# Performance work log

Measured on AMD Instinct MI355X. Metric: run time of the kernel, lower is better.

## Reference

```python
import jax, jax.numpy as jnp
import numpy as np

N = 64
K_CHEB = 5
EPS = 1e-5

# db4 decomposition filters (scaling_filter.mat Lo_D / Hi_D, length 8)
_LO = np.array([-0.010597401784997278, 0.032883011666982945, 0.030841381835986965,
                -0.18703481171888114, -0.02798376941698385, 0.6308807679295904,
                0.7148465705525415, 0.23037781330885523], dtype=np.float32)
_HI = np.array([-0.23037781330885523, 0.7148465705525415, -0.6308807679295904,
                -0.02798376941698385, 0.18703481171888114, 0.030841381835986965,
                0.032883011666982945, -0.010597401784997278], dtype=np.float32)
# torch stores np.flip(filters) and Conv2d does cross-correlation -> use flipped taps here too
_KERN = np.stack([_LO[::-1], _HI[::-1]])[:, None, None, :].copy()  # [2,1,1,8]


def _wavelet_step(x):
    # x: [B, C, 1, W]; circular pad 3 each side, depthwise len-8 conv, stride 2
    p = 3  # filter_length // 2 - 1
    xp = jnp.concatenate([x[..., -p:], x, x[..., :p]], axis=-1)
    b, c, h, wp = xp.shape
    out = jax.lax.conv_general_dilated(
        xp.reshape(b * c, 1, h, wp), jnp.asarray(_KERN), (1, 2), 'VALID',
        dimension_numbers=('NCHW', 'OIHW', 'NCHW'))
    out = out.reshape(b, c, 2, h, -1)
    return out[:, :, 0], out[:, :, 1]  # (approx, detail)


def _cbam(x, fc1, fc2, sa_w):
    # x: [B, 657, 1, 64]; channel attention then spatial attention
    def mlp(v):  # v: [B, C, 1, 1]
        h = jax.nn.relu(jnp.einsum('oc,bchw->bohw', fc1, v))
        return jnp.einsum('oc,bchw->bohw', fc2, h)
    avg = x.mean(axis=(2, 3), keepdims=True)
    mx = x.max(axis=(2, 3), keepdims=True)
    x = x * jax.nn.sigmoid(mlp(avg) + mlp(mx))
    s = jnp.concatenate([x.mean(axis=1, keepdims=True), x.max(axis=1, keepdims=True)], axis=1)
    sa = jax.nn.sigmoid(jax.lax.conv_general_dilated(
        s, sa_w, (1, 1), ((3, 3), (3, 3)), dimension_numbers=('NCHW', 'OIHW', 'NCHW')))
    return x * sa


def _global_edge_weight(w_tril, mask):
    xs, ys = np.tril_indices(N)
    E = jnp.zeros((N, N), w_tril.dtype).at[xs, ys].set(w_tril)
    E = E + E.T - jnp.diag(jnp.diag(E))
    return (E * mask).reshape(-1)


def _norm_adj(edges, w):
    # PyG NewSGConv.norm: add remaining self-loops (fill=1), deg from |w|, sym normalize
    row, col = edges[0], edges[1]
    has_self = jnp.zeros((N,), w.dtype).at[row].add(jnp.where(row == col, 1.0, 0.0)) > 0
    w_self = jnp.where(has_self, 0.0, 1.0).astype(w.dtype)
    deg = jnp.zeros((N,), w.dtype).at[row].add(jnp.abs(w)) + w_self
    dsafe = jnp.where(deg > 0, deg, 1.0)
    dinv = jnp.where(deg > 0, jax.lax.rsqrt(dsafe), 0.0)
    norm = dinv[row] * w * dinv[col]
    A = jnp.zeros((N, N), w.dtype).at[col, row].add(norm)  # out[i] = sum_j A[i,j] x[j]
    return A + jnp.diag(dinv * w_self * dinv)


def _gcn_block(x, A, W, b, g, be):
    # x: [B, N, C_in]; K-hop SGConv propagation, linear, train-mode batchnorm over (B, N)
    for _ in range(K_CHEB):
        x = jnp.einsum('ij,bjc->bic', A, x)
    x = x @ W.T + b
    mean = x.mean(axis=(0, 1))
    var = x.var(axis=(0, 1))
    return (x - mean) * jax.lax.rsqrt(var + EPS) * g + be


def _classify(x, W1, b1, g, be, W2, b2):
    out = x.reshape(x.shape[0], -1) @ W1.T + b1
    out = (out - out.mean(0)) * jax.lax.rsqrt(out.var(0) + EPS) * g + be
    return jax.nn.log_softmax(out @ W2.T + b2, axis=1)


def _forward(x, local_graph_weight, global_mask, ca_fc1, ca_fc2, sa_conv, edge_weight_tril,
             ld_W, ld_b, ld_g, ld_be, ld1_W, ld1_b, ld1_g, ld1_be,
             d_W, d_b, d_g, d_be, d1_W, d1_b, d1_g, d1_be,
             cls_W1, cls_b1, cls_g, cls_be, cls_W2, cls_b2, edges):
    xc = jnp.transpose(x, (0, 3, 2, 1))        # [B, 657, 1, 64]
    xc = _cbam(xc, ca_fc1, ca_fc2, sa_conv)
    xh = jnp.transpose(xc, (0, 3, 2, 1))       # [B, 64, 1, 657]
    # fi = floor(log2(200)) = 7 -> 4 decomposition levels: 657->328->164->82->41
    out1, _gamma = _wavelet_step(xh)
    out2, _beta = _wavelet_step(out1)
    out3, _alpha = _wavelet_step(out2)
    delta, _theta = _wavelet_step(out3)        # [B, 64, 1, 41]
    delta = delta[:, :, 0, :]                  # squeeze -> [B, 64, 41]
    gw = _global_edge_weight(edge_weight_tril, global_mask)
    A_loc = _norm_adj(edges, local_graph_weight)
    A_glb = _norm_adj(edges, gw)
    lf = _gcn_block(delta, A_loc, ld_W, ld_b, ld_g, ld_be)
    lf = _gcn_block(lf, A_loc, ld1_W, ld1_b, ld1_g, ld1_be)
    gf = _gcn_block(delta, A_glb, d_W, d_b, d_g, d_be)
    gf = _gcn_block(gf, A_glb, d1_W, d1_b, d1_g, d1_be)
    feat = jnp.concatenate([lf.mean(-1, keepdims=True), gf.mean(-1, keepdims=True)], axis=2)  # [B,64,2]
    return _classify(feat, cls_W1, cls_b1, cls_g, cls_be, cls_W2, cls_b2)


def setup_inputs() -> dict:
    key = jax.random.key(0)
    ks = iter(jax.random.split(key, 16))
    B = 512
    f32 = jnp.float32
    def rn(shape, s=0.05):
        return jax.random.normal(next(ks), shape, f32) * s
    ii = jnp.arange(N, dtype=jnp.int32)
    edges = jnp.stack([jnp.repeat(ii, N), jnp.tile(ii, N)])  # full 64x64 mesh (incl. self loops)
    return dict(
        x=jax.random.normal(next(ks), (B, N, 1, 657), f32),
        local_graph_weight=jax.random.uniform(next(ks), (N * N,), f32),
        global_mask=jnp.ones((N, N), f32),
        ca_fc1=rn((82, 657)),
        ca_fc2=rn((657, 82)),
        sa_conv=rn((1, 2, 7, 7), 0.1),
        edge_weight_tril=jax.random.uniform(next(ks), (N * (N + 1) // 2,), f32),
        ld_W=rn((16, 41)), ld_b=jnp.zeros(16, f32), ld_g=jnp.ones(16, f32), ld_be=jnp.zeros(16, f32),
        ld1_W=rn((4, 16)), ld1_b=jnp.zeros(4, f32), ld1_g=jnp.ones(4, f32), ld1_be=jnp.zeros(4, f32),
        d_W=rn((16, 41)), d_b=jnp.zeros(16, f32), d_g=jnp.ones(16, f32), d_be=jnp.zeros(16, f32),
        d1_W=rn((4, 16)), d1_b=jnp.zeros(4, f32), d1_g=jnp.ones(4, f32), d1_be=jnp.zeros(4, f32),
        cls_W1=rn((32, 128)), cls_b1=jnp.zeros(32, f32), cls_g=jnp.ones(32, f32), cls_be=jnp.zeros(32, f32),
        cls_W2=rn((2, 32)), cls_b2=jnp.zeros(2, f32),
        edges=edges,
    )


def reference(x, local_graph_weight, global_mask, ca_fc1, ca_fc2, sa_conv, edge_weight_tril,
              ld_W, ld_b, ld_g, ld_be, ld1_W, ld1_b, ld1_g, ld1_be,
              d_W, d_b, d_g, d_be, d1_W, d1_b, d1_g, d1_be,
              cls_W1, cls_b1, cls_g, cls_be, cls_W2, cls_b2, edges):
    return _forward(x, local_graph_weight, global_mask, ca_fc1, ca_fc2, sa_conv, edge_weight_tril,
                    ld_W, ld_b, ld_g, ld_be, ld1_W, ld1_b, ld1_g, ld1_be,
                    d_W, d_b, d_g, d_be, d1_W, d1_b, d1_g, d1_be,
                    cls_W1, cls_b1, cls_g, cls_be, cls_W2, cls_b2, edges)
```

## Files before the change

### kernel.cpp

```cpp
#include <hip/hip_runtime.h>
#include <math.h>

#define NB 512
#define NN 64
#define TL 657
#define LV1 328
#define LV2 164
#define LV3 82
#define LV4 41
#define HID 82
#define BAND 219
#define ST 66

#define WS_M      0
#define WS_ACC    32768
#define WS_SMEAN  36864
#define WS_SMAX   167936
#define WS_FC2T   299008
#define WS_H      514560
#define WS_CSUM   682496
#define WS_CMAX   2028032
#define WS_CATT   3373568
#define WS_Y1     682496
#define WS_DELTA  4876800
#define WS_Y2     4876800
#define WS_OUT1   5925376

#define ACC_Y1 0
#define ACC_Y2 64
#define ACC_O1 80

__device__ __forceinline__ float sigmoidf_(float v){ return 1.0f/(1.0f+expf(-v)); }

__device__ __forceinline__ void wav_level(float* __restrict__ dst, const float* __restrict__ src,
                                          int outL, int inL, int lane){
  const float DLO[8] = {0.23037781330885523f, 0.7148465705525415f, 0.6308807679295904f,
                        -0.02798376941698385f, -0.18703481171888114f, 0.030841381835986965f,
                        0.032883011666982945f, -0.010597401784997278f};
  for (int k=lane; k<outL; k+=64){
    int i0 = 2*k - 3;
    float a = 0.f;
    #pragma unroll
    for (int j=0;j<8;j++){
      int idx = i0 + j;
      idx = (idx < 0) ? idx + inL : ((idx >= inL) ? idx - inL : idx);
      a += src[idx]*DLO[j];
    }
    dst[k] = a;
  }
}

__device__ __forceinline__ void mm8(float* __restrict__ D, int dstride,
                                    const float* __restrict__ A, const float* __restrict__ Bm){
  int tid = threadIdx.x;
  int wv = tid >> 6, lane = tid & 63;
  int i0 = wv*8;
  float acc8[8];
  #pragma unroll
  for (int i=0;i<8;i++) acc8[i]=0.f;
  #pragma unroll
  for (int kc=0; kc<4; kc++){
    float bb[16];
    #pragma unroll
    for (int j=0;j<16;j++) bb[j] = Bm[(kc*16+j)*ST + lane];
    #pragma unroll
    for (int i=0;i<8;i++){
      const float2* ar = (const float2*)&A[(i0+i)*ST + kc*16];
      float s0=0.f, s1=0.f;
      #pragma unroll
      for (int j2=0;j2<8;j2++){
        float2 v = ar[j2];
        s0 += v.x*bb[2*j2]; s1 += v.y*bb[2*j2+1];
      }
      acc8[i] += s0+s1;
    }
  }
  #pragma unroll
  for (int i=0;i<8;i++) D[(i0+i)*dstride + lane] = acc8[i];
}

__global__ __launch_bounds__(512) void k_graph(
    const float* __restrict__ lgw, const float* __restrict__ gmask,
    const float* __restrict__ tril, const int* __restrict__ edges,
    const float* __restrict__ fc2,
    float* __restrict__ Mout, float* __restrict__ fc2T,
    double* __restrict__ acc)
{
  __shared__ float smem[3*NN*ST];
  __shared__ float deg[64], hs[64], dinv[64], wself[64];
  int tid = threadIdx.x;

  if (blockIdx.x >= 2){
    int gi = blockIdx.x - 2;
    int r0 = gi*83;
    int rn = (gi==7) ? (TL - 7*83) : 83;
    for (int i=tid; i<rn*HID; i+=512){
      int r = i / HID, u = i - r*HID;
      smem[u*85 + r] = fc2[(size_t)r0*HID + i];
    }
    __syncthreads();
    for (int j=tid; j<HID*83; j+=512){
      int u = j / 83, c = j - u*83;
      if (c < rn) fc2T[u*TL + r0 + c] = smem[u*85 + c];
    }
    return;
  }

  float* Wbuf = smem;
  float* Amat = smem + NN*ST;
  float* P1   = smem + 2*NN*ST;
  int g = blockIdx.x;
  if (g==0){ for (int i=tid;i<512;i+=512) acc[i]=0.0; }
  for (int e=tid;e<4096;e+=512){
    float w;
    if (g==0) w = lgw[e];
    else {
      int i=e>>6, j=e&63;
      int aa = (i>j)? i:j, bb = (i>j)? j:i;
      w = tril[aa*(aa+1)/2 + bb] * gmask[e];
    }
    Wbuf[e] = w;
  }
  for (int i=tid;i<NN*ST;i+=512) Amat[i] = 0.f;
  if (tid<64){ deg[tid]=0.f; hs[tid]=0.f; }
  __syncthreads();
  {
    int e0 = tid*8;
    int runr = edges[e0];
    float runv = 0.f;
    #pragma unroll 4
    for (int i=0;i<8;i++){
      int e = e0+i;
      int r = edges[e];
      int c = edges[4096+e];
      float w = Wbuf[e];
      if (r != runr){ atomicAdd(&deg[runr], runv); runr = r; runv = 0.f; }
      runv += fabsf(w);
      if (r == c) hs[r] = 1.f;
    }
    atomicAdd(&deg[runr], runv);
  }
  __syncthreads();
  if (tid<64){
    float w_ = (hs[tid] > 0.f) ? 0.f : 1.f;
    float d = deg[tid] + w_;
    dinv[tid] = (d > 0.f) ? rsqrtf(d) : 0.f;
    wself[tid] = w_;
  }
  __syncthreads();
  for (int e=tid;e<4096;e+=512){
    int r = edges[e], c = edges[4096+e];
    float nm = dinv[r]*Wbuf[e]*dinv[c];
    atomicAdd(&Amat[c*ST+r], nm);
  }
  __syncthreads();
  if (tid<64) Amat[tid*ST+tid] += dinv[tid]*wself[tid]*dinv[tid];
  __syncthreads();
  mm8(P1,   ST, Amat, Amat); __syncthreads();
  mm8(Wbuf, ST, P1,   P1);   __syncthreads();
  mm8(&Mout[g*4096], 64, Wbuf, Amat);
}

__global__ __launch_bounds__(256) void k_stats(
    const float* __restrict__ x,
    float* __restrict__ csum, float* __restrict__ cmax)
{
  int tid = threadIdx.x, b = blockIdx.x, band = blockIdx.y;
  if (tid >= BAND) return;
  int col = band*BAND + tid;
  const float* p = x + (size_t)b*NN*TL + col;
  float s = 0.f, m = -INFINITY;
  for (int n=0;n<NN;n+=16){
    float v0 = p[0*TL],  v1 = p[1*TL],  v2 = p[2*TL],  v3 = p[3*TL];
    float v4 = p[4*TL],  v5 = p[5*TL],  v6 = p[6*TL],  v7 = p[7*TL];
    float v8 = p[8*TL],  v9 = p[9*TL],  vA = p[10*TL], vB = p[11*TL];
    float vC = p[12*TL], vD = p[13*TL], vE = p[14*TL], vF = p[15*TL];
    p += 16*TL;
    s += ((v0+v1)+(v2+v3)) + ((v4+v5)+(v6+v7)) + ((v8+v9)+(vA+vB)) + ((vC+vD)+(vE+vF));
    float m01 = fmaxf(fmaxf(v0,v1), fmaxf(v2,v3));
    float m23 = fmaxf(fmaxf(v4,v5), fmaxf(v6,v7));
    float m45 = fmaxf(fmaxf(v8,v9), fmaxf(vA,vB));
    float m67 = fmaxf(fmaxf(vC,vD), fmaxf(vE,vF));
    m = fmaxf(m, fmaxf(fmaxf(m01,m23), fmaxf(m45,m67)));
  }
  csum[(size_t)b*TL + col] = s;
  cmax[(size_t)b*TL + col] = m;
}

__global__ __launch_bounds__(256) void k_mlp1(
    const float* __restrict__ csum, const float* __restrict__ cmax,
    const float* __restrict__ fc1, float* __restrict__ H)
{
  int tid = threadIdx.x, b = blockIdx.x, half = blockIdx.y;
  int wv = tid>>6, lane = tid&63;
  float s[11], m[11];
  #pragma unroll
  for (int i=0;i<11;i++){
    int c = lane + 64*i;
    bool ok = c < TL;
    s[i] = ok ? csum[(size_t)b*TL+c] : 0.f;
    m[i] = ok ? cmax[(size_t)b*TL+c] : 0.f;
  }
  int oend = half*41 + 41; if (oend > HID) oend = HID;
  for (int o = half*41 + wv; o < oend; o += 4){
    const float* fr = fc1 + (size_t)o*TL;
    float a = 0.f, bm = 0.f;
    #pragma unroll
    for (int i=0;i<11;i++){
      int c = lane + 64*i;
      float f = (c<TL) ? fr[c] : 0.f;
      a += f*s[i]; bm += f*m[i];
    }
    #pragma unroll
    for (int off=32;off;off>>=1){
      a  += __shfl_xor(a,off);
      bm += __shfl_xor(bm,off);
    }
    if (lane==0)
      H[(size_t)b*HID + o] = fmaxf(a*(1.0f/64.0f),0.f) + fmaxf(bm,0.f);
  }
}

__global__ __launch_bounds__(256) void k_mlp2(
    const float* __restrict__ H, const float* __restrict__ fc2T,
    float* __restrict__ catt)
{
  __shared__ float h[HID];
  int tid = threadIdx.x, b = blockIdx.x;
  if (tid < HID) h[tid] = H[(size_t)b*HID + tid];
  __syncthreads();
  int c0 = tid, c1 = tid+256, c2 = tid+512;
  bool ok2 = c2 < TL;
  float a0=0.f, a1=0.f, a2=0.f;
  #pragma unroll 2
  for (int u=0;u<HID;u++){
    const float* fr = fc2T + (size_t)u*TL;
    float hv = h[u];
    a0 += fr[c0]*hv;
    a1 += fr[c1]*hv;
    if (ok2) a2 += fr[c2]*hv;
  }
  size_t base = (size_t)b*TL;
  catt[base+c0] = sigmoidf_(a0);
  catt[base+c1] = sigmoidf_(a1);
  if (ok2) catt[base+c2] = sigmoidf_(a2);
}

__global__ __launch_bounds__(256) void k_wav(
    const float* __restrict__ x, const float* __restrict__ catt_g,
    float* __restrict__ delta, float* __restrict__ smean, float* __restrict__ smax)
{
  __shared__ float catt[TL];
  __shared__ float yb[4][TL];
  __shared__ float o1b[4][LV1];
  __shared__ float o2b[4][LV2];
  __shared__ float o3b[4][LV3];
  int tid = threadIdx.x, b = blockIdx.x;
  for (int i=tid;i<TL;i+=256) catt[i] = catt_g[(size_t)b*TL + i];
  __syncthreads();
  int wv = tid>>6, lane = tid&63;
  int n = blockIdx.y*4 + wv;
  float* y  = yb[wv];
  float* p1 = o1b[wv];
  float* p2 = o2b[wv];
  float* p3 = o3b[wv];
  const float DLO[8] = {0.23037781330885523f, 0.7148465705525415f, 0.6308807679295904f,
                        -0.02798376941698385f, -0.18703481171888114f, 0.030841381835986965f,
                        0.032883011666982945f, -0.010597401784997278f};
  const float* row = x + ((size_t)b*NN + n)*TL;
  float ls = 0.f, lm = -INFINITY;
  #pragma unroll
  for (int i=0;i<11;i++){
    int t = lane + 64*i;
    if (t < TL){
      float v = row[t]*catt[t];
      y[t] = v; ls += v; lm = fmaxf(lm,v);
    }
  }
  #pragma unroll
  for (int off=32;off;off>>=1){
    ls += __shfl_xor(ls,off);
    lm = fmaxf(lm, __shfl_xor(lm,off));
  }
  if (lane==0){ smean[b*NN+n] = ls*(1.0f/657.0f); smax[b*NN+n] = lm; }
  wav_level(p1, y,  LV1, TL,  lane);
  wav_level(p2, p1, LV2, LV1, lane);
  wav_level(p3, p2, LV3, LV2, lane);
  if (lane < LV4){
    int i0 = 2*lane - 3;
    float a = 0.f;
    #pragma unroll
    for (int j=0;j<8;j++){
      int idx = i0 + j;
      idx = (idx < 0) ? idx + LV3 : ((idx >= LV3) ? idx - LV3 : idx);
      a += p3[idx]*DLO[j];
    }
    delta[((size_t)b*NN + n)*LV4 + lane] = a;
  }
}

__global__ __launch_bounds__(256) void k_gcn1(
  const float* __restrict__ delta, const float* __restrict__ Mmat,
  const float* __restrict__ smean, const float* __restrict__ smax,
  const float* __restrict__ saw,
  const float* __restrict__ ldW, const float* __restrict__ ldb,
  const float* __restrict__ dW, const float* __restrict__ db2,
  float* __restrict__ Y1, double* __restrict__ acc)
{
  __shared__ float Dl[NN*LV4];
  __shared__ float Tt[NN*16];
  __shared__ float Mm[4096];
  __shared__ float Wl[16*LV4];
  __shared__ float satt[NN];
  __shared__ double red[256];
  int tid=threadIdx.x, b=blockIdx.x;
  if (tid < NN){
    float a = 0.f;
    #pragma unroll
    for (int kw=0;kw<7;kw++){
      int w = tid + kw - 3;
      if (0<=w && w<NN) a += smean[b*NN+w]*saw[21+kw] + smax[b*NN+w]*saw[70+kw];
    }
    satt[tid] = sigmoidf_(a);
  }
  __syncthreads();
  const float* ds = delta + (size_t)b*NN*LV4;
  for (int i=tid;i<NN*LV4;i+=256) Dl[i] = ds[i]*satt[i/LV4];
  for (int g=0; g<2; g++){
    const float* Ws = g ? dW : ldW;
    const float* bs = g ? db2 : ldb;
    for (int i=tid;i<16*LV4;i+=256) Wl[i]=Ws[i];
    for (int i=tid;i<4096;i+=256) Mm[i]=Mmat[g*4096+i];
    __syncthreads();
    for (int e=tid;e<NN*16;e+=256){
      int n=e>>4, o=e&15;
      const float* dr=&Dl[n*LV4];
      const float* wr=&Wl[o*LV4];
      float a=0.f;
      #pragma unroll 8
      for (int c=0;c<LV4;c++) a += dr[c]*wr[c];
      Tt[e]=a;
    }
    __syncthreads();
    float bias = bs[tid&15];
    float ps=0.f, pq=0.f;
    for (int m=0;m<4;m++){
      int e=tid+256*m;
      int n=e>>4, o=e&15;
      float a=bias;
      #pragma unroll 8
      for (int k=0;k<64;k++) a += Mm[n*64+k]*Tt[k*16+o];
      Y1[((size_t)b*NN+n)*32 + g*16 + o] = a;
      ps += a; pq += a*a;
    }
    red[tid]=(double)ps;
    __syncthreads();
    if (tid<16){ double t=0; for (int r=tid;r<256;r+=16) t+=red[r]; atomicAdd(&acc[ACC_Y1+g*32+tid], t); }
    __syncthreads();
    red[tid]=(double)pq;
    __syncthreads();
    if (tid<16){ double t=0; for (int r=tid;r<256;r+=16) t+=red[r]; atomicAdd(&acc[ACC_Y1+g*32+16+tid], t); }
    __syncthreads();
  }
}

__global__ __launch_bounds__(256) void k_gcn2(
  const float* __restrict__ Y1, const float* __restrict__ Mmat,
  const float* __restrict__ ldg, const float* __restrict__ ldbe,
  const float* __restrict__ dg, const float* __restrict__ dbe,
  const float* __restrict__ ld1W, const float* __restrict__ ld1b,
  const float* __restrict__ d1W, const float* __restrict__ d1b,
  float* __restrict__ Y2, double* __restrict__ acc)
{
  __shared__ float Yl[NN*32];
  __shared__ float T2[NN*8];
  __shared__ float Mm[2*4096];
  __shared__ float scl[32], sht[32];
  __shared__ double red[256];
  int tid=threadIdx.x, b=blockIdx.x;
  const float* ys = Y1 + (size_t)b*NN*32;
  for (int i=tid;i<NN*32;i+=256) Yl[i]=ys[i];
  for (int i=tid;i<8192;i+=256) Mm[i]=Mmat[i];
  if (tid<32){
    int g=tid>>4, o=tid&15;
    double s=acc[ACC_Y1+g*32+o], q=acc[ACC_Y1+g*32+16+o];
    double mean=s/32768.0;
    double var=q/32768.0 - mean*mean;
    float gam = g? dg[o] : ldg[o];
    float bet = g? dbe[o] : ldbe[o];
    float sc = gam * rsqrtf((float)var + 1e-5f);
    scl[tid]=sc; sht[tid]=bet - (float)mean*sc;
  }
  __syncthreads();
  for (int i=tid;i<NN*32;i+=256){ int c=i&31; Yl[i]=Yl[i]*scl[c]+sht[c]; }
  __syncthreads();
  for (int e=tid;e<NN*8;e+=256){
    int n=e>>3, c=e&7, g=c>>2, p=c&3;
    const float* w = (g? d1W : ld1W) + p*16;
    const float* yr = &Yl[n*32 + g*16];
    float a=0.f;
    #pragma unroll
    for (int o=0;o<16;o++) a += yr[o]*w[o];
    T2[e]=a;
  }
  __syncthreads();
  float ps=0.f,pq=0.f;
  for (int m=0;m<2;m++){
    int e=tid+256*m;
    int n=e>>3, c=e&7, g=c>>2;
    float a = g? d1b[c&3] : ld1b[c&3];
    const float* mr=&Mm[g*4096+n*64];
    #pragma unroll 8
    for (int k=0;k<64;k++) a += mr[k]*T2[k*8+c];
    Y2[((size_t)b*NN+n)*8 + c] = a;
    ps+=a; pq+=a*a;
  }
  red[tid]=(double)ps; __syncthreads();
  if (tid<8){ double t=0; for (int r=tid;r<256;r+=8) t+=red[r]; atomicAdd(&acc[ACC_Y2 + (tid>>2)*8 + (tid&3)], t); }
  __syncthreads();
  red[tid]=(double)pq; __syncthreads();
  if (tid<8){ double t=0; for (int r=tid;r<256;r+=8) t+=red[r]; atomicAdd(&acc[ACC_Y2 + (tid>>2)*8 + 4 + (tid&3)], t); }
}

__global__ __launch_bounds__(64) void k_featcls(
  const float* __restrict__ Y2,
  const float* __restrict__ ld1g, const float* __restrict__ ld1be,
  const float* __restrict__ d1g, const float* __restrict__ d1be,
  const float* __restrict__ W1, const float* __restrict__ b1,
  float* __restrict__ out1, double* __restrict__ acc)
{
  __shared__ float f[128];
  __shared__ float scl[8], sht[8];
  int tid=threadIdx.x, b=blockIdx.x;
  if (tid<8){
    int g=tid>>2, p=tid&3;
    double s=acc[ACC_Y2+g*8+p], q=acc[ACC_Y2+g*8+4+p];
    double mean=s/32768.0;
    double var=q/32768.0-mean*mean;
    float gam = g? d1g[p]:ld1g[p];
    float bet = g? d1be[p]:ld1be[p];
    float sc = gam*rsqrtf((float)var+1e-5f);
    scl[tid]=sc; sht[tid]=bet-(float)mean*sc;
  }
  __syncthreads();
  {
    const float* yr = Y2 + ((size_t)b*NN+tid)*8;
    float lf=0.f, gf=0.f;
    #pragma unroll
    for (int p=0;p<4;p++){
      lf += yr[p]*scl[p]+sht[p];
      gf += yr[4+p]*scl[4+p]+sht[4+p];
    }
    f[2*tid]   = lf*0.25f;
    f[2*tid+1] = gf*0.25f;
  }
  __syncthreads();
  if (tid<32){
    const float* w = W1 + tid*128;
    float a = b1[tid];
    #pragma unroll 4
    for (int m=0;m<128;m++) a += w[m]*f[m];
    out1[b*32+tid]=a;
    atomicAdd(&acc[ACC_O1+tid], (double)a);
    atomicAdd(&acc[ACC_O1+32+tid], (double)(a*a));
  }
}

__global__ __launch_bounds__(64) void k_cls2(
  const float* __restrict__ out1,
  const float* __restrict__ cg, const float* __restrict__ cbe,
  const float* __restrict__ W2, const float* __restrict__ b2,
  const double* __restrict__ acc, float* __restrict__ out)
{
  __shared__ float v[32];
  __shared__ float z[2];
  int tid=threadIdx.x, b=blockIdx.x;
  if (tid<32){
    double s=acc[ACC_O1+tid], q=acc[ACC_O1+32+tid];
    double mean=s/512.0;
    double var=q/512.0-mean*mean;
    float sc=cg[tid]*rsqrtf((float)var+1e-5f);
    float sh=cbe[tid]-(float)mean*sc;
    v[tid]=out1[b*32+tid]*sc+sh;
  }
  __syncthreads();
  if (tid<2){
    const float* w=W2+tid*32;
    float a=b2[tid];
    #pragma unroll
    for (int j=0;j<32;j++) a += w[j]*v[j];
    z[tid]=a;
  }
  __syncthreads();
  if (tid<2){
    float m=fmaxf(z[0],z[1]);
    float l=m+logf(expf(z[0]-m)+expf(z[1]-m));
    out[b*2+tid]=z[tid]-l;
  }
}

extern "C" void kernel_launch(void* const* d_in, const int* in_sizes, int n_in,
                              void* d_out, int out_size, void* d_ws, size_t ws_size,
                              hipStream_t stream) {
  (void)in_sizes; (void)n_in; (void)out_size; (void)ws_size;
  const float* x     = (const float*)d_in[0];
  const float* lgw   = (const float*)d_in[1];
  const float* gmask = (const float*)d_in[2];
  const float* fc1   = (const float*)d_in[3];
  const float* fc2   = (const float*)d_in[4];
  const float* saw   = (const float*)d_in[5];
  const float* tril  = (const float*)d_in[6];
  const float* ldW   = (const float*)d_in[7];
  const float* ldb   = (const float*)d_in[8];
  const float* ldg   = (const float*)d_in[9];
  const float* ldbe  = (const float*)d_in[10];
  const float* ld1W  = (const float*)d_in[11];
  const float* ld1b  = (const float*)d_in[12];
  const float* ld1g  = (const float*)d_in[13];
  const float* ld1be = (const float*)d_in[14];
  const float* dW    = (const float*)d_in[15];
  const float* db2   = (const float*)d_in[16];
  const float* dg    = (const float*)d_in[17];
  const float* dbe   = (const float*)d_in[18];
  const float* d1W   = (const float*)d_in[19];
  const float* d1b   = (const float*)d_in[20];
  const float* d1g   = (const float*)d_in[21];
  const float* d1be  = (const float*)d_in[22];
  const float* cW1   = (const float*)d_in[23];
  const float* cb1   = (const float*)d_in[24];
  const float* cgam  = (const float*)d_in[25];
  const float* cbet  = (const float*)d_in[26];
  const float* cW2   = (const float*)d_in[27];
  const float* cb2   = (const float*)d_in[28];
  const int*   edges = (const int*)d_in[29];

  char* ws = (char*)d_ws;
  float*  M     = (float*)(ws + WS_M);
  double* acc   = (double*)(ws + WS_ACC);
  float*  smean = (float*)(ws + WS_SMEAN);
  float*  smax  = (float*)(ws + WS_SMAX);
  float*  fc2T  = (float*)(ws + WS_FC2T);
  float*  Hbuf  = (float*)(ws + WS_H);
  float*  csum  = (float*)(ws + WS_CSUM);
  float*  cmax  = (float*)(ws + WS_CMAX);
  float*  catt  = (float*)(ws + WS_CATT);
  float*  Y1    = (float*)(ws + WS_Y1);
  float*  delta = (float*)(ws + WS_DELTA);
  float*  Y2    = (float*)(ws + WS_Y2);
  float*  out1  = (float*)(ws + WS_OUT1);
  float*  out   = (float*)d_out;

  k_graph<<<10, 512, 0, stream>>>(lgw, gmask, tril, edges, fc2, M, fc2T, acc);
  k_stats<<<dim3(NB, 3), 256, 0, stream>>>(x, csum, cmax);
  k_mlp1<<<dim3(NB, 2), 256, 0, stream>>>(csum, cmax, fc1, Hbuf);
  k_mlp2<<<NB, 256, 0, stream>>>(Hbuf, fc2T, catt);
  k_wav<<<dim3(NB, 16), 256, 0, stream>>>(x, catt, delta, smean, smax);
  k_gcn1<<<NB, 256, 0, stream>>>(delta, M, smean, smax, saw, ldW, ldb, dW, db2, Y1, acc);
  k_gcn2<<<NB, 256, 0, stream>>>(Y1, M, ldg, ldbe, dg, dbe, ld1W, ld1b, d1W, d1b, Y2, acc);
  k_featcls<<<NB, 64, 0, stream>>>(Y2, ld1g, ld1be, d1g, d1be, cW1, cb1, out1, acc);
  k_cls2<<<NB, 64, 0, stream>>>(out1, cgam, cbet, cW2, cb2, acc, out);
}
```

Baseline: 188.3 us.

## Fuse graph setup with channel stats and merge the two MLP kernels

The graph/fc2-transpose blocks are merged into the channel-stats kernel as extra blocks of a single launch, and the two channel-attention MLP stages are fused into one kernel that keeps the hidden vector in shared memory. This removes two kernel launches and the global round trip through the hidden buffer. The graph blocks now share a launch with the stats blocks, which may change the overlap, and stats blocks use 512-thread launches with about 329 active threads. The mlp kernel now handles one batch per block rather than splitting the hidden layer across two blocks.

Result: faster. 183.0 us (-2.9%).

```diff
diff --git a/kernel.cpp b/kernel.cpp
--- a/kernel.cpp
+++ b/kernel.cpp
@@ -9,7 +9,6 @@
 #define LV3 82
 #define LV4 41
 #define HID 82
-#define BAND 219
 #define ST 66
 
 #define WS_M      0
@@ -17,7 +16,6 @@
 #define WS_SMEAN  36864
 #define WS_SMAX   167936
 #define WS_FC2T   299008
-#define WS_H      514560
 #define WS_CSUM   682496
 #define WS_CMAX   2028032
 #define WS_CATT   3373568
@@ -79,21 +77,51 @@
   for (int i=0;i<8;i++) D[(i0+i)*dstride + lane] = acc8[i];
 }
 
-__global__ __launch_bounds__(512) void k_graph(
+__global__ __launch_bounds__(512) void k_front(
+    const float* __restrict__ x,
     const float* __restrict__ lgw, const float* __restrict__ gmask,
     const float* __restrict__ tril, const int* __restrict__ edges,
     const float* __restrict__ fc2,
+    float* __restrict__ csum, float* __restrict__ cmax,
     float* __restrict__ Mout, float* __restrict__ fc2T,
     double* __restrict__ acc)
 {
   __shared__ float smem[3*NN*ST];
   __shared__ float deg[64], hs[64], dinv[64], wself[64];
   int tid = threadIdx.x;
-
-  if (blockIdx.x >= 2){
-    int gi = blockIdx.x - 2;
-    int r0 = gi*83;
-    int rn = (gi==7) ? (TL - 7*83) : 83;
+  int bid = blockIdx.x;
+
+  if (bid < 2*NB){
+    int b = bid >> 1, band = bid & 1;
+    int c0   = band ? 329 : 0;
+    int len  = band ? 328 : 329;
+    if (tid >= len) return;
+    int col = c0 + tid;
+    const float* p = x + (size_t)b*NN*TL + col;
+    float s = 0.f, m = -INFINITY;
+    for (int n=0;n<NN;n+=16){
+      float v0 = p[0*TL],  v1 = p[1*TL],  v2 = p[2*TL],  v3 = p[3*TL];
+      float v4 = p[4*TL],  v5 = p[5*TL],  v6 = p[6*TL],  v7 = p[7*TL];
+      float v8 = p[8*TL],  v9 = p[9*TL],  vA = p[10*TL], vB = p[11*TL];
+      float vC = p[12*TL], vD = p[13*TL], vE = p[14*TL], vF = p[15*TL];
+      p += 16*TL;
+      s += ((v0+v1)+(v2+v3)) + ((v4+v5)+(v6+v7)) + ((v8+v9)+(vA+vB)) + ((vC+vD)+(vE+vF));
+      float m01 = fmaxf(fmaxf(v0,v1), fmaxf(v2,v3));
+      float m23 = fmaxf(fmaxf(v4,v5), fmaxf(v6,v7));
+      float m45 = fmaxf(fmaxf(v8,v9), fmaxf(vA,vB));
+      float m67 = fmaxf(fmaxf(vC,vD), fmaxf(vE,vF));
+      m = fmaxf(m, fmaxf(fmaxf(m01,m23), fmaxf(m45,m67)));
+    }
+    csum[(size_t)b*TL + col] = s;
+    cmax[(size_t)b*TL + col] = m;
+    return;
+  }
+
+  int gi = bid - 2*NB;
+  if (gi >= 2){
+    int t8 = gi - 2;
+    int r0 = t8*83;
+    int rn = (t8==7) ? (TL - 7*83) : 83;
     for (int i=tid; i<rn*HID; i+=512){
       int r = i / HID, u = i - r*HID;
       smem[u*85 + r] = fc2[(size_t)r0*HID + i];
@@ -109,8 +137,8 @@
   float* Wbuf = smem;
   float* Amat = smem + NN*ST;
   float* P1   = smem + 2*NN*ST;
-  int g = blockIdx.x;
-  if (g==0){ for (int i=tid;i<512;i+=512) acc[i]=0.0; }
+  int g = gi;
+  if (g==0 && tid<512) acc[tid]=0.0;
   for (int e=tid;e<4096;e+=512){
     float w;
     if (g==0) w = lgw[e];
@@ -161,55 +189,30 @@
   mm8(&Mout[g*4096], 64, Wbuf, Amat);
 }
 
-__global__ __launch_bounds__(256) void k_stats(
-    const float* __restrict__ x,
-    float* __restrict__ csum, float* __restrict__ cmax)
-{
-  int tid = threadIdx.x, b = blockIdx.x, band = blockIdx.y;
-  if (tid >= BAND) return;
-  int col = band*BAND + tid;
-  const float* p = x + (size_t)b*NN*TL + col;
-  float s = 0.f, m = -INFINITY;
-  for (int n=0;n<NN;n+=16){
-    float v0 = p[0*TL],  v1 = p[1*TL],  v2 = p[2*TL],  v3 = p[3*TL];
-    float v4 = p[4*TL],  v5 = p[5*TL],  v6 = p[6*TL],  v7 = p[7*TL];
-    float v8 = p[8*TL],  v9 = p[9*TL],  vA = p[10*TL], vB = p[11*TL];
-    float vC = p[12*TL], vD = p[13*TL], vE = p[14*TL], vF = p[15*TL];
-    p += 16*TL;
-    s += ((v0+v1)+(v2+v3)) + ((v4+v5)+(v6+v7)) + ((v8+v9)+(vA+vB)) + ((vC+vD)+(vE+vF));
-    float m01 = fmaxf(fmaxf(v0,v1), fmaxf(v2,v3));
-    float m23 = fmaxf(fmaxf(v4,v5), fmaxf(v6,v7));
-    float m45 = fmaxf(fmaxf(v8,v9), fmaxf(vA,vB));
-    float m67 = fmaxf(fmaxf(vC,vD), fmaxf(vE,vF));
-    m = fmaxf(m, fmaxf(fmaxf(m01,m23), fmaxf(m45,m67)));
-  }
-  csum[(size_t)b*TL + col] = s;
-  cmax[(size_t)b*TL + col] = m;
-}
-
-__global__ __launch_bounds__(256) void k_mlp1(
+__global__ __launch_bounds__(512) void k_mlp(
     const float* __restrict__ csum, const float* __restrict__ cmax,
-    const float* __restrict__ fc1, float* __restrict__ H)
-{
-  int tid = threadIdx.x, b = blockIdx.x, half = blockIdx.y;
+    const float* __restrict__ fc1, const float* __restrict__ fc2T,
+    float* __restrict__ catt)
+{
+  __shared__ float cs[TL], cm[TL];
+  __shared__ float h[HID];
+  int tid = threadIdx.x, b = blockIdx.x;
+  for (int i=tid;i<TL;i+=512){
+    cs[i] = csum[(size_t)b*TL + i];
+    cm[i] = cmax[(size_t)b*TL + i];
+  }
+  __syncthreads();
   int wv = tid>>6, lane = tid&63;
-  float s[11], m[11];
-  #pragma unroll
-  for (int i=0;i<11;i++){
-    int c = lane + 64*i;
-    bool ok = c < TL;
-    s[i] = ok ? csum[(size_t)b*TL+c] : 0.f;
-    m[i] = ok ? cmax[(size_t)b*TL+c] : 0.f;
-  }
-  int oend = half*41 + 41; if (oend > HID) oend = HID;
-  for (int o = half*41 + wv; o < oend; o += 4){
+  for (int o=wv; o<HID; o+=8){
     const float* fr = fc1 + (size_t)o*TL;
     float a = 0.f, bm = 0.f;
     #pragma unroll
     for (int i=0;i<11;i++){
       int c = lane + 64*i;
-      float f = (c<TL) ? fr[c] : 0.f;
-      a += f*s[i]; bm += f*m[i];
+      if (c < TL){
+        float f = fr[c];
+        a += f*cs[c]; bm += f*cm[c];
+      }
     }
     #pragma unroll
     for (int off=32;off;off>>=1){
@@ -217,33 +220,15 @@
       bm += __shfl_xor(bm,off);
     }
     if (lane==0)
-      H[(size_t)b*HID + o] = fmaxf(a*(1.0f/64.0f),0.f) + fmaxf(bm,0.f);
-  }
-}
-
-__global__ __launch_bounds__(256) void k_mlp2(
-    const float* __restrict__ H, const float* __restrict__ fc2T,
-    float* __restrict__ catt)
-{
-  __shared__ float h[HID];
-  int tid = threadIdx.x, b = blockIdx.x;
-  if (tid < HID) h[tid] = H[(size_t)b*HID + tid];
-  __syncthreads();
-  int c0 = tid, c1 = tid+256, c2 = tid+512;
-  bool ok2 = c2 < TL;
-  float a0=0.f, a1=0.f, a2=0.f;
-  #pragma unroll 2
-  for (int u=0;u<HID;u++){
-    const float* fr = fc2T + (size_t)u*TL;
-    float hv = h[u];
-    a0 += fr[c0]*hv;
-    a1 += fr[c1]*hv;
-    if (ok2) a2 += fr[c2]*hv;
-  }
-  size_t base = (size_t)b*TL;
-  catt[base+c0] = sigmoidf_(a0);
-  catt[base+c1] = sigmoidf_(a1);
-  if (ok2) catt[base+c2] = sigmoidf_(a2);
+      h[o] = fmaxf(a*(1.0f/64.0f),0.f) + fmaxf(bm,0.f);
+  }
+  __syncthreads();
+  for (int c=tid;c<TL;c+=512){
+    float a=0.f;
+    #pragma unroll 4
+    for (int u=0;u<HID;u++) a += fc2T[(size_t)u*TL + c]*h[u];
+    catt[(size_t)b*TL + c] = sigmoidf_(a);
+  }
 }
 
 __global__ __launch_bounds__(256) void k_wav(
@@ -540,7 +525,6 @@
   float*  smean = (float*)(ws + WS_SMEAN);
   float*  smax  = (float*)(ws + WS_SMAX);
   float*  fc2T  = (float*)(ws + WS_FC2T);
-  float*  Hbuf  = (float*)(ws + WS_H);
   float*  csum  = (float*)(ws + WS_CSUM);
   float*  cmax  = (float*)(ws + WS_CMAX);
   float*  catt  = (float*)(ws + WS_CATT);
@@ -550,10 +534,9 @@
   float*  out1  = (float*)(ws + WS_OUT1);
   float*  out   = (float*)d_out;
 
-  k_graph<<<10, 512, 0, stream>>>(lgw, gmask, tril, edges, fc2, M, fc2T, acc);
-  k_stats<<<dim3(NB, 3), 256, 0, stream>>>(x, csum, cmax);
-  k_mlp1<<<dim3(NB, 2), 256, 0, stream>>>(csum, cmax, fc1, Hbuf);
-  k_mlp2<<<NB, 256, 0, stream>>>(Hbuf, fc2T, catt);
+  k_front<<<2*NB + 10, 512, 0, stream>>>(x, lgw, gmask, tril, edges, fc2,
+                                         csum, cmax, M, fc2T, acc);
+  k_mlp<<<NB, 512, 0, stream>>>(csum, cmax, fc1, fc2T, catt);
   k_wav<<<dim3(NB, 16), 256, 0, stream>>>(x, catt, delta, smean, smax);
   k_gcn1<<<NB, 256, 0, stream>>>(delta, M, smean, smax, saw, ldW, ldb, dW, db2, Y1, acc);
   k_gcn2<<<NB, 256, 0, stream>>>(Y1, M, ldg, ldbe, dg, dbe, ld1W, ld1b, d1W, d1b, Y2, acc);
```
